# Kernel tuning notes

Hardware: AMD Instinct MI355X
Metric: run time of the kernel (lower is better)

## Reference

```python
import jax, jax.numpy as jnp
import numpy as np

N = 50000      # nodes
E = 800000     # edges in normalized A (incl. self loops)
DIN = 128      # input_dim
DOUT = 64      # output_dim
BN_EPS = 1e-5
SLOPE = 0.01   # LeakyReLU default negative slope


def setup_inputs() -> dict:
    key = jax.random.key(0)
    ks = jax.random.split(key, 10)
    H = jax.random.normal(ks[0], (N, DIN), dtype=jnp.float32)
    rows = jax.random.randint(ks[1], (E,), 0, N, dtype=jnp.int32)
    cols = jax.random.randint(ks[2], (E,), 0, N, dtype=jnp.int32)
    # values of the symmetrically normalized adjacency (precomputed in __init__)
    vals = jax.random.uniform(ks[3], (E,), dtype=jnp.float32)
    # BatchNorm1d params/buffers (eval mode: use running stats)
    gamma = 1.0 + 0.1 * jax.random.normal(ks[4], (DIN,), dtype=jnp.float32)
    beta = 0.1 * jax.random.normal(ks[5], (DIN,), dtype=jnp.float32)
    run_mean = 0.1 * jax.random.normal(ks[6], (DIN,), dtype=jnp.float32)
    run_var = 0.5 + jax.random.uniform(ks[7], (DIN,), dtype=jnp.float32)
    # Linear(input_dim, output_dim)
    W = jax.random.normal(ks[8], (DIN, DOUT), dtype=jnp.float32) / np.sqrt(DIN)
    b = 0.01 * jax.random.normal(ks[9], (DOUT,), dtype=jnp.float32)
    return dict(H=H, rows=rows, cols=cols, vals=vals, gamma=gamma, beta=beta,
                run_mean=run_mean, run_var=run_var, W=W, b=b)


def reference(H, rows, cols, vals, gamma, beta, run_mean, run_var, W, b):
    # F.normalize: L2 row normalization with eps=1e-12
    norm = jnp.maximum(jnp.linalg.norm(H, axis=1, keepdims=True), 1e-12)
    Hn = H / norm
    # BatchNorm1d (eval: running stats); dropout is identity in eval
    scale = gamma * jax.lax.rsqrt(run_var + BN_EPS)
    Hb = (Hn - run_mean) * scale + beta
    # Linear projection [N, DIN] @ [DIN, DOUT]
    X = Hb @ W + b
    # SpMM: out[r] = sum_{e: rows[e]==r} vals[e] * X[cols[e]]
    msgs = vals[:, None] * X[cols]            # [E, DOUT] gather + scale
    out = jax.ops.segment_sum(msgs, rows, num_segments=N)
    # LeakyReLU
    return jnp.where(out >= 0, out, SLOPE * out)
```

## Files before the change

### kernel.cpp

```cpp
#include <hip/hip_runtime.h>
#include <hip/hip_fp16.h>

#define N_NODES 50000
#define E_EDGES 800000
#define DIN 128
#define DOUT 64
#define NBUK 784
#define NSEG 8
#define SEGCAP 256
#define WINCAP (NSEG * SEGCAP)
#define CHUNK 2048
#define NBLKA 391
#define KXBLK 782
#define ASTRIDE 136
#define EVLCAP 1792

typedef short short8 __attribute__((ext_vector_type(8)));
typedef float f32x4 __attribute__((ext_vector_type(4)));

static __device__ __forceinline__ short f2bf(float f)
{
    union { float f; unsigned u; } x{f};
    const unsigned r = x.u + 0x7FFFu + ((x.u >> 16) & 1u);
    return (short)(r >> 16);
}

union SMemFront {
    struct { short A[64][ASTRIDE]; } x;
    struct {
        int lhist[NBUK]; int lstart[NBUK]; int lcur[NBUK]; int gbase[NBUK];
        int scn[256];
        unsigned lbinVC[CHUNK];
        unsigned short lbinBR[CHUNK];
    } a;
};

__global__ __launch_bounds__(256) void k_w(
    const float* __restrict__ W, unsigned short* __restrict__ Wb)
{
    const int s = blockIdx.x * 256 + threadIdx.x;
    const int k0 = s >> 8, f = (s >> 6) & 3, l = s & 63;
    const int kbase = k0 * 32 + (l >> 4) * 8;
    const int n = f * 16 + (l & 15);
    unsigned short tmp[8];
#pragma unroll
    for (int j = 0; j < 8; ++j)
        tmp[j] = (unsigned short)f2bf(W[(size_t)(kbase + j) * DOUT + n]);
    *(uint4*)(Wb + (size_t)s * 8) = *(const uint4*)tmp;
}

__global__ __launch_bounds__(256) void k_front(
    const float* __restrict__ H, const float* __restrict__ gamma,
    const float* __restrict__ beta, const float* __restrict__ mean,
    const float* __restrict__ var, const unsigned short* __restrict__ Wb,
    const float* __restrict__ bias, unsigned short* __restrict__ X16,
    const int* __restrict__ rows, const int* __restrict__ cols,
    const float* __restrict__ vals, int* __restrict__ gcursor,
    unsigned* __restrict__ midVC, unsigned char* __restrict__ midR)
{
    __shared__ SMemFront sm;
    const int t = threadIdx.x;

    if (blockIdx.x < NBLKA) {
        const int seg = blockIdx.x & (NSEG - 1);
        const int e0 = blockIdx.x * CHUNK;
        const int nC = min(CHUNK, E_EDGES - e0);

        for (int i = t; i < NBUK; i += 256) sm.a.lhist[i] = 0;
        __syncthreads();

        unsigned prVC[8];
        unsigned short prBR[8];
#pragma unroll
        for (int k = 0; k < 8; ++k) {
            const int e = e0 + k * 256 + t;
            if (e < E_EDGES) {
                const int r = rows[e];
                const unsigned hv = __half_as_ushort(__float2half(vals[e]));
                prVC[k] = (hv << 16) | (unsigned)cols[e];
                prBR[k] = (unsigned short)r;
                atomicAdd(&sm.a.lhist[r >> 6], 1);
            } else {
                prBR[k] = 0xFFFFu;
            }
        }
        __syncthreads();

        const int b0 = t * 4;
        int h0 = 0, h1 = 0, h2 = 0, h3 = 0;
        if (b0 < NBUK) {
            h0 = sm.a.lhist[b0];     h1 = sm.a.lhist[b0 + 1];
            h2 = sm.a.lhist[b0 + 2]; h3 = sm.a.lhist[b0 + 3];
        }
        const int lsum = h0 + h1 + h2 + h3;
        sm.a.scn[t] = lsum;
        __syncthreads();
        for (int o = 1; o < 256; o <<= 1) {
            int u = 0;
            if (t >= o) u = sm.a.scn[t - o];
            __syncthreads();
            sm.a.scn[t] += u;
            __syncthreads();
        }
        if (b0 < NBUK) {
            int ex = sm.a.scn[t] - lsum;
            const int s0 = ex, s1 = s0 + h0, s2 = s1 + h1, s3 = s2 + h2;
            sm.a.lstart[b0] = s0;     sm.a.lcur[b0] = s0;
            sm.a.lstart[b0 + 1] = s1; sm.a.lcur[b0 + 1] = s1;
            sm.a.lstart[b0 + 2] = s2; sm.a.lcur[b0 + 2] = s2;
            sm.a.lstart[b0 + 3] = s3; sm.a.lcur[b0 + 3] = s3;
            sm.a.gbase[b0]     = b0 * WINCAP + seg * SEGCAP +
                (h0 ? atomicAdd(&gcursor[b0 * NSEG + seg], h0) : 0);
            sm.a.gbase[b0 + 1] = (b0 + 1) * WINCAP + seg * SEGCAP +
                (h1 ? atomicAdd(&gcursor[(b0 + 1) * NSEG + seg], h1) : 0);
            sm.a.gbase[b0 + 2] = (b0 + 2) * WINCAP + seg * SEGCAP +
                (h2 ? atomicAdd(&gcursor[(b0 + 2) * NSEG + seg], h2) : 0);
            sm.a.gbase[b0 + 3] = (b0 + 3) * WINCAP + seg * SEGCAP +
                (h3 ? atomicAdd(&gcursor[(b0 + 3) * NSEG + seg], h3) : 0);
        }
        __syncthreads();

#pragma unroll
        for (int k = 0; k < 8; ++k) {
            if (prBR[k] != 0xFFFFu) {
                const int bk = prBR[k] >> 6;
                const int pos = atomicAdd(&sm.a.lcur[bk], 1);
                sm.a.lbinVC[pos] = prVC[k];
                sm.a.lbinBR[pos] = prBR[k];
            }
        }
        __syncthreads();

        for (int i = t; i < nC; i += 256) {
            const unsigned short br = sm.a.lbinBR[i];
            const int bk = br >> 6;
            const int g = sm.a.gbase[bk] + (i - sm.a.lstart[bk]);
            if (g < bk * WINCAP + (seg + 1) * SEGCAP) {
                midVC[g] = sm.a.lbinVC[i];
                midR[g] = (unsigned char)(br & 63);
            }
        }
        return;
    }

    const int l = t & 63, wv = t >> 6;
    const int R0 = (blockIdx.x - NBLKA) * 64;

    {
        const int rloc = t >> 2, sub = t & 3;
        const int r = R0 + rloc;
        float4 h[8];
        if (r < N_NODES) {
            const float4* hp = (const float4*)(H + (size_t)r * DIN + sub * 32);
#pragma unroll
            for (int i = 0; i < 8; ++i) h[i] = hp[i];
        } else {
#pragma unroll
            for (int i = 0; i < 8; ++i) h[i] = make_float4(0.f, 0.f, 0.f, 0.f);
        }
        float ss = 0.f;
#pragma unroll
        for (int i = 0; i < 8; ++i)
            ss += h[i].x * h[i].x + h[i].y * h[i].y + h[i].z * h[i].z + h[i].w * h[i].w;
        ss += __shfl_xor(ss, 1, 64);
        ss += __shfl_xor(ss, 2, 64);
        const float inv = 1.0f / fmaxf(sqrtf(ss), 1e-12f);

        const float4* gp = (const float4*)(gamma + sub * 32);
        const float4* bp = (const float4*)(beta  + sub * 32);
        const float4* mp = (const float4*)(mean  + sub * 32);
        const float4* vp = (const float4*)(var   + sub * 32);
#pragma unroll
        for (int i = 0; i < 8; ++i) {
            const float4 g4 = gp[i], b4 = bp[i], m4 = mp[i], v4 = vp[i];
            const float s0 = g4.x * rsqrtf(v4.x + 1e-5f);
            const float s1 = g4.y * rsqrtf(v4.y + 1e-5f);
            const float s2 = g4.z * rsqrtf(v4.z + 1e-5f);
            const float s3 = g4.w * rsqrtf(v4.w + 1e-5f);
            const float e0 = h[i].x * inv * s0 + (b4.x - m4.x * s0);
            const float e1 = h[i].y * inv * s1 + (b4.y - m4.y * s1);
            const float e2 = h[i].z * inv * s2 + (b4.z - m4.z * s2);
            const float e3 = h[i].w * inv * s3 + (b4.w - m4.w * s3);
            const unsigned u0 = (unsigned short)f2bf(e0) | ((unsigned)(unsigned short)f2bf(e1) << 16);
            const unsigned u1 = (unsigned short)f2bf(e2) | ((unsigned)(unsigned short)f2bf(e3) << 16);
            *(uint2*)&sm.x.A[rloc][sub * 32 + i * 4] = make_uint2(u0, u1);
        }
    }

    const int ml = l & 15, q = l >> 4;
    f32x4 c0, c1, c2, c3;
    {
        const float b0 = bias[ml],      b1 = bias[16 + ml];
        const float b2 = bias[32 + ml], b3 = bias[48 + ml];
        c0 = f32x4{b0, b0, b0, b0};
        c1 = f32x4{b1, b1, b1, b1};
        c2 = f32x4{b2, b2, b2, b2};
        c3 = f32x4{b3, b3, b3, b3};
    }
    __syncthreads();

#pragma unroll
    for (int k0 = 0; k0 < 4; ++k0) {
        const short8 a  = *(const short8*)&sm.x.A[wv * 16 + ml][k0 * 32 + q * 8];
        const short8 b0 = *(const short8*)(Wb + (size_t)((k0 * 4 + 0) * 64 + l) * 8);
        const short8 b1 = *(const short8*)(Wb + (size_t)((k0 * 4 + 1) * 64 + l) * 8);
        const short8 b2 = *(const short8*)(Wb + (size_t)((k0 * 4 + 2) * 64 + l) * 8);
        const short8 b3 = *(const short8*)(Wb + (size_t)((k0 * 4 + 3) * 64 + l) * 8);
        c0 = __builtin_amdgcn_mfma_f32_16x16x32_bf16(a, b0, c0, 0, 0, 0);
        c1 = __builtin_amdgcn_mfma_f32_16x16x32_bf16(a, b1, c1, 0, 0, 0);
        c2 = __builtin_amdgcn_mfma_f32_16x16x32_bf16(a, b2, c2, 0, 0, 0);
        c3 = __builtin_amdgcn_mfma_f32_16x16x32_bf16(a, b3, c3, 0, 0, 0);
    }

    __syncthreads();
    unsigned short* otile = (unsigned short*)&sm.x.A[0][0];
#pragma unroll
    for (int i = 0; i < 4; ++i) {
        const int r = wv * 16 + q * 4 + i;
        otile[r * 64 + ml]      = __half_as_ushort(__float2half(c0[i]));
        otile[r * 64 + 16 + ml] = __half_as_ushort(__float2half(c1[i]));
        otile[r * 64 + 32 + ml] = __half_as_ushort(__float2half(c2[i]));
        otile[r * 64 + 48 + ml] = __half_as_ushort(__float2half(c3[i]));
    }
    __syncthreads();
#pragma unroll
    for (int rep = 0; rep < 2; ++rep) {
        const int id = rep * 256 + t;
        const int row = id >> 3;
        const int off = (id & 7) * 8;
        if (R0 + row < N_NODES)
            *(uint4*)(X16 + (size_t)(R0 + row) * DOUT + off) =
                *(const uint4*)&otile[row * 64 + off];
    }
}

__global__ __launch_bounds__(512) void k_back(
    const int* __restrict__ gcursor, const unsigned* __restrict__ midVC,
    const unsigned char* __restrict__ midR,
    const unsigned short* __restrict__ X16, float* __restrict__ out)
{
    __shared__ int lhist[64], scn[64], lcur[64], lrowS[64], lrowE[64];
    __shared__ unsigned evl[EVLCAP];
    const int t = threadIdx.x;
    const int q = blockIdx.x;

    if (t < 64) lhist[t] = 0;
    __syncthreads();

    for (int s = 0; s < NSEG; ++s) {
        const int cnt = min(gcursor[q * NSEG + s], SEGCAP);
        const int sbase = q * WINCAP + s * SEGCAP;
        for (int i = t; i < cnt; i += 512)
            atomicAdd(&lhist[midR[sbase + i]], 1);
    }
    __syncthreads();

    const int v = (t < 64) ? lhist[t] : 0;
    if (t < 64) scn[t] = v;
    __syncthreads();
    for (int o = 1; o < 64; o <<= 1) {
        int u = 0;
        if (t < 64 && t >= o) u = scn[t - o];
        __syncthreads();
        if (t < 64) scn[t] += u;
        __syncthreads();
    }
    if (t < 64) {
        const int ex = scn[t] - v;
        lcur[t] = ex;
        lrowS[t] = ex;
        lrowE[t] = ex + v;
    }
    __syncthreads();

    for (int s = 0; s < NSEG; ++s) {
        const int cnt = min(gcursor[q * NSEG + s], SEGCAP);
        const int sbase = q * WINCAP + s * SEGCAP;
        for (int i = t; i < cnt; i += 512) {
            const int lr = midR[sbase + i];
            const int pos = atomicAdd(&lcur[lr], 1);
            if (pos < EVLCAP) evl[pos] = midVC[sbase + i];
        }
    }
    __syncthreads();

    const int lane = t & 63;
    const int wv   = t >> 6;
    const int sub  = lane & 15;
    const int g4   = lane >> 4;
#pragma unroll 1
    for (int k = 0; k < 8; ++k) {
        const int rr = wv * 8 + k;
        const int grow = (q << 6) + rr;
        const int s  = lrowS[rr];
        const int e2 = min(lrowE[rr], EVLCAP);
        float a0 = 0.f, a1 = 0.f, a2 = 0.f, a3 = 0.f;
        int e = s + g4;
        for (; e + 12 < e2; e += 16) {
            const unsigned u0 = evl[e];
            const unsigned u1 = evl[e + 4];
            const unsigned u2 = evl[e + 8];
            const unsigned u3 = evl[e + 12];
            const uint2 x0 = *(const uint2*)(X16 + (u0 & 0xFFFFu) * DOUT + sub * 4);
            const uint2 x1 = *(const uint2*)(X16 + (u1 & 0xFFFFu) * DOUT + sub * 4);
            const uint2 x2 = *(const uint2*)(X16 + (u2 & 0xFFFFu) * DOUT + sub * 4);
            const uint2 x3 = *(const uint2*)(X16 + (u3 & 0xFFFFu) * DOUT + sub * 4);
            const float v0 = __half2float(__ushort_as_half((unsigned short)(u0 >> 16)));
            const float v1 = __half2float(__ushort_as_half((unsigned short)(u1 >> 16)));
            const float v2 = __half2float(__ushort_as_half((unsigned short)(u2 >> 16)));
            const float v3 = __half2float(__ushort_as_half((unsigned short)(u3 >> 16)));
            const float2 f00 = __half22float2(*(const __half2*)&x0.x);
            const float2 f01 = __half22float2(*(const __half2*)&x0.y);
            const float2 f10 = __half22float2(*(const __half2*)&x1.x);
            const float2 f11 = __half22float2(*(const __half2*)&x1.y);
            const float2 f20 = __half22float2(*(const __half2*)&x2.x);
            const float2 f21 = __half22float2(*(const __half2*)&x2.y);
            const float2 f30 = __half22float2(*(const __half2*)&x3.x);
            const float2 f31 = __half22float2(*(const __half2*)&x3.y);
            a0 = fmaf(v0, f00.x, a0); a1 = fmaf(v0, f00.y, a1);
            a2 = fmaf(v0, f01.x, a2); a3 = fmaf(v0, f01.y, a3);
            a0 = fmaf(v1, f10.x, a0); a1 = fmaf(v1, f10.y, a1);
            a2 = fmaf(v1, f11.x, a2); a3 = fmaf(v1, f11.y, a3);
            a0 = fmaf(v2, f20.x, a0); a1 = fmaf(v2, f20.y, a1);
            a2 = fmaf(v2, f21.x, a2); a3 = fmaf(v2, f21.y, a3);
            a0 = fmaf(v3, f30.x, a0); a1 = fmaf(v3, f30.y, a1);
            a2 = fmaf(v3, f31.x, a2); a3 = fmaf(v3, f31.y, a3);
        }
        for (; e < e2; e += 4) {
            const unsigned u = evl[e];
            const uint2 x = *(const uint2*)(X16 + (u & 0xFFFFu) * DOUT + sub * 4);
            const float vv = __half2float(__ushort_as_half((unsigned short)(u >> 16)));
            const float2 f0 = __half22float2(*(const __half2*)&x.x);
            const float2 f1 = __half22float2(*(const __half2*)&x.y);
            a0 = fmaf(vv, f0.x, a0); a1 = fmaf(vv, f0.y, a1);
            a2 = fmaf(vv, f1.x, a2); a3 = fmaf(vv, f1.y, a3);
        }
        a0 += __shfl_xor(a0, 16, 64); a1 += __shfl_xor(a1, 16, 64);
        a2 += __shfl_xor(a2, 16, 64); a3 += __shfl_xor(a3, 16, 64);
        a0 += __shfl_xor(a0, 32, 64); a1 += __shfl_xor(a1, 32, 64);
        a2 += __shfl_xor(a2, 32, 64); a3 += __shfl_xor(a3, 32, 64);
        if (g4 == 0 && grow < N_NODES) {
            float4 r;
            r.x = (a0 >= 0.f) ? a0 : 0.01f * a0;
            r.y = (a1 >= 0.f) ? a1 : 0.01f * a1;
            r.z = (a2 >= 0.f) ? a2 : 0.01f * a2;
            r.w = (a3 >= 0.f) ? a3 : 0.01f * a3;
            *(float4*)(out + (size_t)grow * DOUT + sub * 4) = r;
        }
    }
}

extern "C" void kernel_launch(void* const* d_in, const int* in_sizes, int n_in,
                              void* d_out, int out_size, void* d_ws, size_t ws_size,
                              hipStream_t stream)
{
    const float* H     = (const float*)d_in[0];
    const int*   rows  = (const int*)  d_in[1];
    const int*   cols  = (const int*)  d_in[2];
    const float* vals  = (const float*)d_in[3];
    const float* gamma = (const float*)d_in[4];
    const float* beta  = (const float*)d_in[5];
    const float* mean  = (const float*)d_in[6];
    const float* var   = (const float*)d_in[7];
    const float* W     = (const float*)d_in[8];
    const float* bias  = (const float*)d_in[9];
    float* out = (float*)d_out;

    char* ws = (char*)d_ws;
    unsigned short* X16     = (unsigned short*)(ws);
    int*            gcursor = (int*)          (ws +  6400000);
    unsigned short* Wb      = (unsigned short*)(ws + 6425088);
    unsigned*       midVC   = (unsigned*)     (ws +  6441472);
    unsigned char*  midR    = (unsigned char*)(ws + 12864000);

    hipMemsetAsync(gcursor, 0, NBUK * NSEG * sizeof(int), stream);

    k_w<<<4, 256, 0, stream>>>(W, Wb);
    k_front<<<NBLKA + KXBLK, 256, 0, stream>>>(H, gamma, beta, mean, var, Wb,
                                               bias, X16, rows, cols, vals,
                                               gcursor, midVC, midR);
    k_back<<<NBUK, 512, 0, stream>>>(gcursor, midVC, midR, X16, out);
}
```

Before: 152.5 us.

## Scatter edges directly to global as packed uint2, drop LDS staging buffer

The binning blocks no longer stage edges in a shared-memory bucket-sorted buffer before writing. Each thread now writes its record straight to the global bucket slot it claims through the shared cursor atomic. The value/col word and the local row now travel together as one uint2 record instead of two separate arrays. The block-wide LDS scan becomes a wavefront shuffle scan plus a 4-entry cross-wave sum, which cuts barriers and shrinks LDS so occupancy can rise. The trade-off is less coalesced global writes and an 8-byte record (instead of 5 bytes) read in the back kernel.

```diff
diff --git a/kernel.cpp b/kernel.cpp
--- a/kernel.cpp
+++ b/kernel.cpp
@@ -29,9 +29,7 @@
     struct { short A[64][ASTRIDE]; } x;
     struct {
         int lhist[NBUK]; int lstart[NBUK]; int lcur[NBUK]; int gbase[NBUK];
-        int scn[256];
-        unsigned lbinVC[CHUNK];
-        unsigned short lbinBR[CHUNK];
+        int wsum[4];
     } a;
 };
 
@@ -56,7 +54,7 @@
     const float* __restrict__ bias, unsigned short* __restrict__ X16,
     const int* __restrict__ rows, const int* __restrict__ cols,
     const float* __restrict__ vals, int* __restrict__ gcursor,
-    unsigned* __restrict__ midVC, unsigned char* __restrict__ midR)
+    uint2* __restrict__ midE)
 {
     __shared__ SMemFront sm;
     const int t = threadIdx.x;
@@ -64,13 +62,13 @@
     if (blockIdx.x < NBLKA) {
         const int seg = blockIdx.x & (NSEG - 1);
         const int e0 = blockIdx.x * CHUNK;
-        const int nC = min(CHUNK, E_EDGES - e0);
+        const int lane = t & 63, wvx = t >> 6;
 
         for (int i = t; i < NBUK; i += 256) sm.a.lhist[i] = 0;
         __syncthreads();
 
         unsigned prVC[8];
-        unsigned short prBR[8];
+        unsigned short prR[8];
 #pragma unroll
         for (int k = 0; k < 8; ++k) {
             const int e = e0 + k * 256 + t;
@@ -78,10 +76,10 @@
                 const int r = rows[e];
                 const unsigned hv = __half_as_ushort(__float2half(vals[e]));
                 prVC[k] = (hv << 16) | (unsigned)cols[e];
-                prBR[k] = (unsigned short)r;
+                prR[k] = (unsigned short)r;
                 atomicAdd(&sm.a.lhist[r >> 6], 1);
             } else {
-                prBR[k] = 0xFFFFu;
+                prR[k] = 0xFFFFu;
             }
         }
         __syncthreads();
@@ -93,17 +91,20 @@
             h2 = sm.a.lhist[b0 + 2]; h3 = sm.a.lhist[b0 + 3];
         }
         const int lsum = h0 + h1 + h2 + h3;
-        sm.a.scn[t] = lsum;
-        __syncthreads();
-        for (int o = 1; o < 256; o <<= 1) {
-            int u = 0;
-            if (t >= o) u = sm.a.scn[t - o];
-            __syncthreads();
-            sm.a.scn[t] += u;
-            __syncthreads();
-        }
+        int incl = lsum;
+#pragma unroll
+        for (int o = 1; o < 64; o <<= 1) {
+            const int u = __shfl_up(incl, o, 64);
+            if (lane >= o) incl += u;
+        }
+        if (lane == 63) sm.a.wsum[wvx] = incl;
+        __syncthreads();
+        int wbase = 0;
+#pragma unroll
+        for (int i = 0; i < 4; ++i)
+            if (i < wvx) wbase += sm.a.wsum[i];
         if (b0 < NBUK) {
-            int ex = sm.a.scn[t] - lsum;
+            const int ex = wbase + incl - lsum;
             const int s0 = ex, s1 = s0 + h0, s2 = s1 + h1, s3 = s2 + h2;
             sm.a.lstart[b0] = s0;     sm.a.lcur[b0] = s0;
             sm.a.lstart[b0 + 1] = s1; sm.a.lcur[b0 + 1] = s1;
@@ -122,22 +123,12 @@
 
 #pragma unroll
         for (int k = 0; k < 8; ++k) {
-            if (prBR[k] != 0xFFFFu) {
-                const int bk = prBR[k] >> 6;
+            if (prR[k] != 0xFFFFu) {
+                const int bk = prR[k] >> 6;
                 const int pos = atomicAdd(&sm.a.lcur[bk], 1);
-                sm.a.lbinVC[pos] = prVC[k];
-                sm.a.lbinBR[pos] = prBR[k];
-            }
-        }
-        __syncthreads();
-
-        for (int i = t; i < nC; i += 256) {
-            const unsigned short br = sm.a.lbinBR[i];
-            const int bk = br >> 6;
-            const int g = sm.a.gbase[bk] + (i - sm.a.lstart[bk]);
-            if (g < bk * WINCAP + (seg + 1) * SEGCAP) {
-                midVC[g] = sm.a.lbinVC[i];
-                midR[g] = (unsigned char)(br & 63);
+                const int g = sm.a.gbase[bk] + (pos - sm.a.lstart[bk]);
+                if (g < bk * WINCAP + (seg + 1) * SEGCAP)
+                    midE[g] = make_uint2(prVC[k], (unsigned)(prR[k] & 63));
             }
         }
         return;
@@ -235,8 +226,7 @@
 }
 
 __global__ __launch_bounds__(512) void k_back(
-    const int* __restrict__ gcursor, const unsigned* __restrict__ midVC,
-    const unsigned char* __restrict__ midR,
+    const int* __restrict__ gcursor, const uint2* __restrict__ midE,
     const unsigned short* __restrict__ X16, float* __restrict__ out)
 {
     __shared__ int lhist[64], scn[64], lcur[64], lrowS[64], lrowE[64];
@@ -251,7 +241,7 @@
         const int cnt = min(gcursor[q * NSEG + s], SEGCAP);
         const int sbase = q * WINCAP + s * SEGCAP;
         for (int i = t; i < cnt; i += 512)
-            atomicAdd(&lhist[midR[sbase + i]], 1);
+            atomicAdd(&lhist[midE[sbase + i].y], 1);
     }
     __syncthreads();
 
@@ -277,9 +267,9 @@
         const int cnt = min(gcursor[q * NSEG + s], SEGCAP);
         const int sbase = q * WINCAP + s * SEGCAP;
         for (int i = t; i < cnt; i += 512) {
-            const int lr = midR[sbase + i];
-            const int pos = atomicAdd(&lcur[lr], 1);
-            if (pos < EVLCAP) evl[pos] = midVC[sbase + i];
+            const uint2 rec = midE[sbase + i];
+            const int pos = atomicAdd(&lcur[rec.y], 1);
+            if (pos < EVLCAP) evl[pos] = rec.x;
         }
     }
     __syncthreads();
@@ -370,14 +360,13 @@
     unsigned short* X16     = (unsigned short*)(ws);
     int*            gcursor = (int*)          (ws +  6400000);
     unsigned short* Wb      = (unsigned short*)(ws + 6425088);
-    unsigned*       midVC   = (unsigned*)     (ws +  6441472);
-    unsigned char*  midR    = (unsigned char*)(ws + 12864000);
+    uint2*          midE    = (uint2*)        (ws +  6441472);
 
     hipMemsetAsync(gcursor, 0, NBUK * NSEG * sizeof(int), stream);
 
     k_w<<<4, 256, 0, stream>>>(W, Wb);
     k_front<<<NBLKA + KXBLK, 256, 0, stream>>>(H, gamma, beta, mean, var, Wb,
                                                bias, X16, rows, cols, vals,
-                                               gcursor, midVC, midR);
-    k_back<<<NBUK, 512, 0, stream>>>(gcursor, midVC, midR, X16, out);
-}
+                                               gcursor, midE);
+    k_back<<<NBUK, 512, 0, stream>>>(gcursor, midE, X16, out);
+}
```

Result: no change. 153.1 us (+0.4%).
